# Optimization experiments

Measured on AMD Instinct MI355X. Metric: run time of the kernel, lower is better.

Reference implementation:

```python
import jax, jax.numpy as jnp
import numpy as np

N = 50000       # nodes
E = 800000      # edges (avg degree 16)
IN = 256        # input features
HEADS = 4
D = 32          # per-head dim (hidden_channels/heads = 128/4)
HID = HEADS * D # 128
OUT = 64        # out_channels, last layer has 1 head
SLOPE = 0.2     # DGL GATConv LeakyReLU negative slope


def setup_inputs() -> dict:
    key = jax.random.key(0)
    ks = jax.random.split(key, 11)
    s = 0.05
    return {
        "x": jax.random.normal(ks[0], (N, IN), jnp.float32),
        "W1": jax.random.normal(ks[1], (IN, HID), jnp.float32) * s,
        "al1": jax.random.normal(ks[2], (HEADS, D), jnp.float32) * s,
        "ar1": jax.random.normal(ks[3], (HEADS, D), jnp.float32) * s,
        "b1": jnp.zeros((HID,), jnp.float32),
        "W2": jax.random.normal(ks[4], (HID, OUT), jnp.float32) * s,
        "al2": jax.random.normal(ks[5], (1, OUT), jnp.float32) * s,
        "ar2": jax.random.normal(ks[6], (1, OUT), jnp.float32) * s,
        "b2": jnp.zeros((OUT,), jnp.float32),
        "src": jax.random.randint(ks[7], (E,), 0, N),
        "dst": jax.random.randint(ks[8], (E,), 0, N),
    }


def gat_conv(h, W, al, ar, b, src, dst, heads, d):
    # h: [N, F_in]; projects, computes edge attention, edge-softmax over dst,
    # scatter-reduce aggregation. Matches dglnn.GATConv (bias, no residual).
    feat = (h @ W).reshape(-1, heads, d)              # [N, H, D]
    el = jnp.einsum('nhd,hd->nh', feat, al)           # [N, H]
    er = jnp.einsum('nhd,hd->nh', feat, ar)           # [N, H]
    e = jax.nn.leaky_relu(el[src] + er[dst], SLOPE)   # [E, H] edge scores
    # edge softmax over incoming edges of each dst node
    m = jax.ops.segment_max(e, dst, num_segments=N)   # [N, H]
    ee = jnp.exp(e - m[dst])                          # [E, H]
    z = jax.ops.segment_sum(ee, dst, num_segments=N)  # [N, H]
    a = ee / z[dst]                                   # [E, H]
    msg = feat[src] * a[:, :, None]                   # [E, H, D] gather + weight
    out = jax.ops.segment_sum(msg, dst, num_segments=N)  # [N, H, D]
    return out + b.reshape(heads, d)


def reference(x, W1, al1, ar1, b1, W2, al2, ar2, b2, src, dst):
    h = gat_conv(x, W1, al1, ar1, b1, src, dst, HEADS, D)   # [N, 4, 32]
    h = jax.nn.relu(h).reshape(N, HID)                      # activation; dropout=identity (eval)
    h = gat_conv(h, W2, al2, ar2, b2, src, dst, 1, OUT)     # [N, 1, 64]
    return h.reshape(N, OUT)
```

## Files before the change

kernel.cpp:

```cpp
#include <hip/hip_runtime.h>
#include <math.h>

#define NN   50000
#define EE   800000
#define INF_ 256
#define HID  128
#define OUTF 64
#define DCAP 96
#define SLOPE 0.2f
#define G1B  782
#define NB   391
#define NCH  196
#define CHCAP 6144

typedef __attribute__((ext_vector_type(8))) short short8v;
typedef __attribute__((ext_vector_type(4))) float f32x4;

__device__ __forceinline__ float lrelu(float x) { return x > 0.f ? x : SLOPE * x; }
__device__ __forceinline__ float4 lrelu4(float4 v) {
  v.x = lrelu(v.x); v.y = lrelu(v.y); v.z = lrelu(v.z); v.w = lrelu(v.w); return v;
}
__device__ __forceinline__ unsigned short f2bf(float x) {
  unsigned int u = __float_as_uint(x);
  unsigned int r = (u + 0x7FFFu + ((u >> 16) & 1u)) >> 16;
  return (unsigned short)r;
}

__global__ __launch_bounds__(256) void prep_k(const int* __restrict__ src,
                                              const int* __restrict__ dst,
                                              int* __restrict__ cursor,
                                              int* __restrict__ packed,
                                              const float* __restrict__ W1,
                                              const float* __restrict__ W2,
                                              unsigned short* __restrict__ W1T,
                                              unsigned short* __restrict__ W2T) {
  int t = threadIdx.x;
  if (blockIdx.x >= NB) {
    int id = (blockIdx.x - NB) * 256 + t;
    if (id < 32768) {
      int k = id >> 7, c = id & 127;
      W1T[c * 256 + k] = f2bf(W1[k * 128 + c]);
    } else {
      int i2 = id - 32768;
      if (i2 < 8192) {
        int k = i2 >> 6, c = i2 & 63;
        W2T[c * 128 + k] = f2bf(W2[i2]);
      }
    }
    return;
  }
  __shared__ int h[NCH];
  __shared__ int cur[NCH];
  int b = blockIdx.x;
  if (t < NCH) h[t] = 0;
  __syncthreads();
  const int4* d4p = (const int4*)dst;
  const int4* s4p = (const int4*)src;
  int4 d4[2], s4[2];
  bool val[2];
#pragma unroll
  for (int it = 0; it < 2; ++it) {
    int qi = b * 512 + it * 256 + t;
    val[it] = qi < EE / 4;
    if (val[it]) {
      d4[it] = d4p[qi];
      s4[it] = s4p[qi];
      atomicAdd(&h[d4[it].x >> 8], 1);
      atomicAdd(&h[d4[it].y >> 8], 1);
      atomicAdd(&h[d4[it].z >> 8], 1);
      atomicAdd(&h[d4[it].w >> 8], 1);
    }
  }
  __syncthreads();
  if (t < NCH) {
    int c = h[t];
    cur[t] = t * CHCAP + ((c > 0) ? atomicAdd(&cursor[t], c) : 0);
  }
  __syncthreads();
#pragma unroll
  for (int it = 0; it < 2; ++it) {
    if (val[it]) {
      int p, c, lim;
      c = d4[it].x >> 8; lim = (c + 1) * CHCAP;
      p = atomicAdd(&cur[c], 1); if (p < lim) packed[p] = (s4[it].x << 8) | (d4[it].x & 255);
      c = d4[it].y >> 8; lim = (c + 1) * CHCAP;
      p = atomicAdd(&cur[c], 1); if (p < lim) packed[p] = (s4[it].y << 8) | (d4[it].y & 255);
      c = d4[it].z >> 8; lim = (c + 1) * CHCAP;
      p = atomicAdd(&cur[c], 1); if (p < lim) packed[p] = (s4[it].z << 8) | (d4[it].z & 255);
      c = d4[it].w >> 8; lim = (c + 1) * CHCAP;
      p = atomicAdd(&cur[c], 1); if (p < lim) packed[p] = (s4[it].w << 8) | (d4[it].w & 255);
    }
  }
}

__global__ __launch_bounds__(256) void cg1_k(const int* __restrict__ packed,
                                             const int* __restrict__ cursor,
                                             int* __restrict__ adj,
                                             int* __restrict__ rowptr,
                                             int* __restrict__ cnt,
                                             const float* __restrict__ x,
                                             const unsigned short* __restrict__ W1T,
                                             unsigned short* __restrict__ featb,
                                             const float* __restrict__ al,
                                             const float* __restrict__ ar,
                                             float* __restrict__ el,
                                             float* __restrict__ er) {
  __shared__ char smem[32768];
  int t = threadIdx.x;

  if (blockIdx.x < NCH) {
    int* pk  = (int*)smem;
    int* h   = (int*)(smem + 24576);
    int* sc  = (int*)(smem + 25600);
    int* cur = (int*)(smem + 26624);
    int b = blockIdx.x;
    int base = b * CHCAP;
    int len = cursor[b]; if (len > CHCAP) len = CHCAP;
    h[t] = 0;
    __syncthreads();
    for (int i = t; i < len; i += 256) {
      int v = packed[base + i];
      pk[i] = v;
      atomicAdd(&h[v & 255], 1);
    }
    __syncthreads();
    int v0 = h[t];
    sc[t] = v0;
    __syncthreads();
    for (int off = 1; off < 256; off <<= 1) {
      int add = (t >= off) ? sc[t - off] : 0;
      __syncthreads();
      sc[t] += add;
      __syncthreads();
    }
    int excl = sc[t] - v0;
    int node = b * 256 + t;
    if (node < NN) { cnt[node] = v0; rowptr[node] = base + excl; }
    cur[t] = excl;
    __syncthreads();
    for (int i = t; i < len; i += 256) {
      int v = pk[i];
      int p = atomicAdd(&cur[v & 255], 1);
      adj[base + p] = v & 0xFFFFFF00;
    }
    return;
  }

  unsigned short* As = (unsigned short*)smem;
  unsigned short* Bs = (unsigned short*)(smem + 16384);
  int lane = t & 63, wid = t >> 6;
  int n0 = (blockIdx.x - NCH) * 64;
  int wr = wid * 16;

  f32x4 acc[2][4];
#pragma unroll
  for (int m = 0; m < 2; ++m)
#pragma unroll
    for (int n = 0; n < 4; ++n) acc[m][n] = (f32x4){0.f, 0.f, 0.f, 0.f};

  for (int pass = 0; pass < 2; ++pass) {
    int k0 = pass * 128;
#pragma unroll
    for (int it = 0; it < 8; ++it) {
      int f = it * 256 + t;
      int row = f >> 5;
      int c4  = f & 31;
      int grow = n0 + row;
      float4 v = make_float4(0.f, 0.f, 0.f, 0.f);
      if (grow < NN) v = *(const float4*)&x[grow * INF_ + k0 + c4 * 4];
      ushort4 b4;
      b4.x = f2bf(v.x); b4.y = f2bf(v.y); b4.z = f2bf(v.z); b4.w = f2bf(v.w);
      int byte = row * 256 + c4 * 8;
      byte ^= (row & 15) << 4;
      *(ushort4*)((char*)As + byte) = b4;
    }
#pragma unroll
    for (int ch = 0; ch < 2; ++ch) {
#pragma unroll
      for (int it = 0; it < 4; ++it) {
        int f = it * 256 + t;
        int c  = f >> 4;
        int k8 = f & 15;
        uint4 v = *(const uint4*)&W1T[(ch * 64 + c) * 256 + k0 + k8 * 8];
        int byte = c * 256 + k8 * 16;
        byte ^= (c & 15) << 4;
        *(uint4*)((char*)Bs + byte) = v;
      }
      __syncthreads();
#pragma unroll
      for (int ks = 0; ks < 4; ++ks) {
        int kb = ks * 64 + (lane >> 4) * 16;
        int arow = wr + (lane & 15);
        int abyte = (arow * 256 + kb) ^ ((arow & 15) << 4);
        short8v a = *(const short8v*)((const char*)As + abyte);
#pragma unroll
        for (int n = 0; n < 4; ++n) {
          int c = n * 16 + (lane & 15);
          int bbyte = (c * 256 + kb) ^ ((c & 15) << 4);
          short8v b = *(const short8v*)((const char*)Bs + bbyte);
          acc[ch][n] = __builtin_amdgcn_mfma_f32_16x16x32_bf16(a, b, acc[ch][n], 0, 0, 0);
        }
      }
      __syncthreads();
    }
  }
#pragma unroll
  for (int ch = 0; ch < 2; ++ch) {
    int rbase = wr + (lane >> 4) * 4;
#pragma unroll
    for (int r = 0; r < 4; ++r)
#pragma unroll
      for (int n = 0; n < 4; ++n)
        As[(rbase + r) * 128 + ch * 64 + n * 16 + (lane & 15)] = f2bf(acc[ch][n][r]);
  }
  __syncthreads();
#pragma unroll
  for (int it = 0; it < 4; ++it) {
    int id = it * 256 + t;
    int row = id >> 4, c8 = id & 15;
    int grow = n0 + row;
    if (grow < NN)
      *(uint4*)&featb[grow * HID + c8 * 8] = *(const uint4*)&As[row * 128 + c8 * 8];
  }
  {
    int row = t >> 2, hh = t & 3;
    int grow = n0 + row;
    float pe = 0.f, pr = 0.f;
#pragma unroll
    for (int d = 0; d < 16; ++d) {
      unsigned int u = *(const unsigned int*)&As[row * 128 + hh * 32 + d * 2];
      float f0 = __uint_as_float(u << 16);
      float f1 = __uint_as_float(u & 0xFFFF0000u);
      float2 a2 = *(const float2*)&al[hh * 32 + d * 2];
      float2 r2 = *(const float2*)&ar[hh * 32 + d * 2];
      pe += f0 * a2.x + f1 * a2.y;
      pr += f0 * r2.x + f1 * r2.y;
    }
    if (grow < NN) { el[grow * 4 + hh] = pe; er[grow * 4 + hh] = pr; }
  }
}

__global__ __launch_bounds__(256) void agg1_k(const unsigned short* __restrict__ featb,
                                              const float* __restrict__ el1,
                                              const float* __restrict__ er1,
                                              const float* __restrict__ b1,
                                              const int* __restrict__ cnt,
                                              const int* __restrict__ rowptr,
                                              const int* __restrict__ adj,
                                              unsigned short* __restrict__ houtb) {
  __shared__ float ee[4][DCAP * 4];
  int wid = threadIdx.x >> 6, lane = threadIdx.x & 63;
  int n = blockIdx.x * 4 + wid;
  int deg = cnt[n]; if (deg > DCAP) deg = DCAP;
  const int* bk = adj + rowptr[n];
  float4 er = *(const float4*)(er1 + n * 4);
  int hl = lane >> 4;
  int m64 = deg < 64 ? deg : 64;
  int myoff = (lane < m64) ? bk[lane] : -1;
  const char* fb = (const char*)featb;
  int lb = lane * 4;

  float4 e4my = make_float4(0.f, 0.f, 0.f, 0.f);
  if (myoff >= 0 && deg <= 64)
    e4my = *(const float4*)((const char*)el1 + (myoff >> 4));
  unsigned int upre[16];
#pragma unroll
  for (int k = 0; k < 16; ++k) {
    int o = __shfl(myoff, k);
    upre[k] = *(const unsigned int*)(fb + ((k < m64) ? o : 0) + lb);
  }
  __builtin_amdgcn_sched_barrier(0);

  if (deg <= 64) {
    float4 ex = make_float4(0.f, 0.f, 0.f, 0.f);
    if (myoff >= 0) {
      float4 sc = lrelu4(make_float4(e4my.x + er.x, e4my.y + er.y,
                                     e4my.z + er.z, e4my.w + er.w));
      ex = make_float4(__expf(sc.x), __expf(sc.y), __expf(sc.z), __expf(sc.w));
    }
    float4 zs = ex;
#pragma unroll
    for (int off = 1; off < 64; off <<= 1) {
      zs.x += __shfl_xor(zs.x, off); zs.y += __shfl_xor(zs.y, off);
      zs.z += __shfl_xor(zs.z, off); zs.w += __shfl_xor(zs.w, off);
    }
    if (myoff >= 0) {
      float4 w = make_float4(ex.x / zs.x, ex.y / zs.y, ex.z / zs.z, ex.w / zs.w);
      *(float4*)&ee[wid][lane * 4] = w;
    }
  } else {
    float4 mx = make_float4(-INFINITY, -INFINITY, -INFINITY, -INFINITY);
    for (int j = lane; j < deg; j += 64) {
      int o = bk[j];
      float4 e4 = *(const float4*)((const char*)el1 + (o >> 4));
      float4 sc = lrelu4(make_float4(e4.x + er.x, e4.y + er.y, e4.z + er.z, e4.w + er.w));
      mx.x = fmaxf(mx.x, sc.x); mx.y = fmaxf(mx.y, sc.y);
      mx.z = fmaxf(mx.z, sc.z); mx.w = fmaxf(mx.w, sc.w);
    }
#pragma unroll
    for (int off = 1; off < 64; off <<= 1) {
      mx.x = fmaxf(mx.x, __shfl_xor(mx.x, off));
      mx.y = fmaxf(mx.y, __shfl_xor(mx.y, off));
      mx.z = fmaxf(mx.z, __shfl_xor(mx.z, off));
      mx.w = fmaxf(mx.w, __shfl_xor(mx.w, off));
    }
    float4 zs = make_float4(0.f, 0.f, 0.f, 0.f);
    for (int j = lane; j < deg; j += 64) {
      int o = bk[j];
      float4 e4 = *(const float4*)((const char*)el1 + (o >> 4));
      float4 sc = lrelu4(make_float4(e4.x + er.x, e4.y + er.y, e4.z + er.z, e4.w + er.w));
      float4 ex = make_float4(__expf(sc.x - mx.x), __expf(sc.y - mx.y),
                              __expf(sc.z - mx.z), __expf(sc.w - mx.w));
      *(float4*)&ee[wid][j * 4] = ex;
      zs.x += ex.x; zs.y += ex.y; zs.z += ex.z; zs.w += ex.w;
    }
#pragma unroll
    for (int off = 1; off < 64; off <<= 1) {
      zs.x += __shfl_xor(zs.x, off); zs.y += __shfl_xor(zs.y, off);
      zs.z += __shfl_xor(zs.z, off); zs.w += __shfl_xor(zs.w, off);
    }
    float4 iz = make_float4(1.f / zs.x, 1.f / zs.y, 1.f / zs.z, 1.f / zs.w);
    for (int j = lane; j < deg; j += 64) {
      float4 t = *(const float4*)&ee[wid][j * 4];
      t.x *= iz.x; t.y *= iz.y; t.z *= iz.z; t.w *= iz.w;
      *(float4*)&ee[wid][j * 4] = t;
    }
  }

  float acc0 = 0.f, acc1 = 0.f;
#pragma unroll
  for (int k = 0; k < 16; ++k) {
    float w = (k < m64) ? ee[wid][k * 4 + hl] : 0.f;
    acc0 += __uint_as_float(upre[k] << 16) * w;
    acc1 += __uint_as_float(upre[k] & 0xFFFF0000u) * w;
  }
  int j = 16;
  for (; j + 16 <= m64; j += 16) {
    unsigned int u[16];
#pragma unroll
    for (int q = 0; q < 16; ++q) {
      int o = __shfl(myoff, j + q);
      u[q] = *(const unsigned int*)(fb + o + lb);
    }
#pragma unroll
    for (int q = 0; q < 16; ++q) {
      float w = ee[wid][(j + q) * 4 + hl];
      acc0 += __uint_as_float(u[q] << 16) * w;
      acc1 += __uint_as_float(u[q] & 0xFFFF0000u) * w;
    }
  }
  for (; j + 4 <= m64; j += 4) {
    unsigned int u[4];
#pragma unroll
    for (int q = 0; q < 4; ++q) {
      int o = __shfl(myoff, j + q);
      u[q] = *(const unsigned int*)(fb + o + lb);
    }
#pragma unroll
    for (int q = 0; q < 4; ++q) {
      float w = ee[wid][(j + q) * 4 + hl];
      acc0 += __uint_as_float(u[q] << 16) * w;
      acc1 += __uint_as_float(u[q] & 0xFFFF0000u) * w;
    }
  }
  for (; j < m64; ++j) {
    int o = __shfl(myoff, j);
    unsigned int u = *(const unsigned int*)(fb + o + lb);
    float w = ee[wid][j * 4 + hl];
    acc0 += __uint_as_float(u << 16) * w; acc1 += __uint_as_float(u & 0xFFFF0000u) * w;
  }
  for (; j < deg; ++j) {
    int o = bk[j];
    unsigned int u = *(const unsigned int*)(fb + o + lb);
    float w = ee[wid][j * 4 + hl];
    acc0 += __uint_as_float(u << 16) * w; acc1 += __uint_as_float(u & 0xFFFF0000u) * w;
  }
  float2 bb = *(const float2*)&b1[lane * 2];
  float o0 = fmaxf(acc0 + bb.x, 0.f);
  float o1 = fmaxf(acc1 + bb.y, 0.f);
  unsigned int p = (unsigned int)f2bf(o0) | ((unsigned int)f2bf(o1) << 16);
  *(unsigned int*)&houtb[n * HID + lane * 2] = p;
}

__global__ __launch_bounds__(256) void gemm2s_mfma(const unsigned short* __restrict__ hb,
                                                   const unsigned short* __restrict__ W2T,
                                                   unsigned short* __restrict__ f2b,
                                                   const float* __restrict__ al2,
                                                   const float* __restrict__ ar2,
                                                   float* __restrict__ el2,
                                                   float* __restrict__ er2) {
  __shared__ char smem[32768];
  __shared__ float pel[64][4], per_[64][4];
  unsigned short* As = (unsigned short*)smem;
  unsigned short* Bs = (unsigned short*)(smem + 16384);
  int t = threadIdx.x, lane = t & 63, wid = t >> 6;
  int n0 = blockIdx.x * 64;
  f32x4 acc[4];
#pragma unroll
  for (int n = 0; n < 4; ++n) acc[n] = (f32x4){0.f, 0.f, 0.f, 0.f};

#pragma unroll
  for (int it = 0; it < 4; ++it) {
    int id = it * 256 + t;
    int row = id >> 4, c8 = id & 15;
    int grow = n0 + row;
    uint4 v = make_uint4(0, 0, 0, 0);
    if (grow < NN) v = *(const uint4*)&hb[grow * HID + c8 * 8];
    int byte = row * 256 + c8 * 16;
    byte ^= (row & 15) << 4;
    *(uint4*)((char*)As + byte) = v;
  }
#pragma unroll
  for (int it = 0; it < 4; ++it) {
    int id = it * 256 + t;
    int row = id >> 4, c8 = id & 15;
    uint4 v = *(const uint4*)&W2T[row * 128 + c8 * 8];
    int byte = row * 256 + c8 * 16;
    byte ^= (row & 15) << 4;
    *(uint4*)((char*)Bs + byte) = v;
  }
  __syncthreads();
  int wr = wid * 16;
#pragma unroll
  for (int ks = 0; ks < 4; ++ks) {
    int kb = ks * 64 + (lane >> 4) * 16;
    int arow = wr + (lane & 15);
    int abyte = (arow * 256 + kb) ^ ((arow & 15) << 4);
    short8v a = *(const short8v*)((const char*)As + abyte);
#pragma unroll
    for (int n = 0; n < 4; ++n) {
      int c = n * 16 + (lane & 15);
      int bbyte = (c * 256 + kb) ^ ((c & 15) << 4);
      short8v b = *(const short8v*)((const char*)Bs + bbyte);
      acc[n] = __builtin_amdgcn_mfma_f32_16x16x32_bf16(a, b, acc[n], 0, 0, 0);
    }
  }
  __syncthreads();
  float* stg = (float*)smem;
  unsigned short* sB = (unsigned short*)(smem + 16640);
  int rloc = wr + (lane >> 4) * 4;
#pragma unroll
  for (int r = 0; r < 4; ++r) {
#pragma unroll
    for (int n = 0; n < 4; ++n) {
      int col = n * 16 + (lane & 15);
      float v = acc[n][r];
      stg[(rloc + r) * 65 + col] = v;
      sB[(rloc + r) * 64 + col] = f2bf(v);
    }
  }
  __syncthreads();
#pragma unroll
  for (int it = 0; it < 2; ++it) {
    int id = it * 256 + t;
    int row = id >> 3, c8 = id & 7;
    int grow = n0 + row;
    if (grow < NN)
      *(uint4*)&f2b[grow * OUTF + c8 * 8] = *(const uint4*)&sB[row * 64 + c8 * 8];
  }
  {
    int row = t >> 2, seg = t & 3;
    float pe = 0.f, pr = 0.f;
#pragma unroll
    for (int d = 0; d < 16; ++d) {
      int c = seg * 16 + d;
      float f = stg[row * 65 + c];
      pe += f * al2[c];
      pr += f * ar2[c];
    }
    pel[row][seg] = pe; per_[row][seg] = pr;
  }
  __syncthreads();
  if (t < 64) {
    int grow = n0 + t;
    if (grow < NN) {
      el2[grow] = pel[t][0] + pel[t][1] + pel[t][2] + pel[t][3];
      er2[grow] = per_[t][0] + per_[t][1] + per_[t][2] + per_[t][3];
    }
  }
}

__global__ __launch_bounds__(256) void agg2_k(const unsigned short* __restrict__ f2b,
                                              const float* __restrict__ el2,
                                              const float* __restrict__ er2,
                                              const float* __restrict__ b2,
                                              const int* __restrict__ cnt,
                                              const int* __restrict__ rowptr,
                                              const int* __restrict__ adj,
                                              float* __restrict__ out) {
  __shared__ float ee[4][DCAP];
  int wid = threadIdx.x >> 6, lane = threadIdx.x & 63;
  int n = blockIdx.x * 4 + wid;
  int deg = cnt[n]; if (deg > DCAP) deg = DCAP;
  const int* bk = adj + rowptr[n];
  float er = er2[n];
  int m64 = deg < 64 ? deg : 64;
  int myoff = (lane < m64) ? bk[lane] : -1;
  int half = lane >> 5, c2 = (lane & 31) * 2;
  const char* fb = (const char*)f2b;

  float elmy = 0.f;
  if (myoff >= 0 && deg <= 64)
    elmy = *(const float*)((const char*)el2 + (myoff >> 6));
  unsigned int upre[8];
#pragma unroll
  for (int s = 0; s < 8; ++s) {
    int je = s * 2 + half;
    int o = __shfl(myoff, je);
    upre[s] = *(const unsigned int*)(fb + ((je < m64) ? (o >> 1) : 0) + c2 * 2);
  }
  __builtin_amdgcn_sched_barrier(0);

  if (deg <= 64) {
    float ex = (myoff >= 0) ? __expf(lrelu(elmy + er)) : 0.f;
    float zs = ex;
#pragma unroll
    for (int off = 1; off < 64; off <<= 1) zs += __shfl_xor(zs, off);
    if (myoff >= 0) ee[wid][lane] = ex / zs;
  } else {
    float mx = -INFINITY;
    for (int j = lane; j < deg; j += 64) {
      int o = bk[j];
      mx = fmaxf(mx, lrelu(*(const float*)((const char*)el2 + (o >> 6)) + er));
    }
#pragma unroll
    for (int off = 1; off < 64; off <<= 1) mx = fmaxf(mx, __shfl_xor(mx, off));
    float zs = 0.f;
    for (int j = lane; j < deg; j += 64) {
      int o = bk[j];
      float ex = __expf(lrelu(*(const float*)((const char*)el2 + (o >> 6)) + er) - mx);
      ee[wid][j] = ex;
      zs += ex;
    }
#pragma unroll
    for (int off = 1; off < 64; off <<= 1) zs += __shfl_xor(zs, off);
    float iz = 1.f / zs;
    for (int j = lane; j < deg; j += 64) ee[wid][j] *= iz;
  }

  float acc0 = 0.f, acc1 = 0.f;
#pragma unroll
  for (int s = 0; s < 8; ++s) {
    int je = s * 2 + half;
    float w = (je < m64) ? ee[wid][je] : 0.f;
    acc0 += __uint_as_float(upre[s] << 16) * w;
    acc1 += __uint_as_float(upre[s] & 0xFFFF0000u) * w;
  }
  int j = 16;
  for (; j + 16 <= deg; j += 16) {
    unsigned int u[8]; float w[8];
#pragma unroll
    for (int q = 0; q < 8; ++q) {
      int je = j + q * 2 + half;
      int os = __shfl(myoff, je < 64 ? je : 63);
      int o = (je < 64) ? os : bk[je];
      u[q] = *(const unsigned int*)(fb + (o >> 1) + c2 * 2);
      w[q] = ee[wid][je];
    }
#pragma unroll
    for (int q = 0; q < 8; ++q) {
      acc0 += __uint_as_float(u[q] << 16) * w[q];
      acc1 += __uint_as_float(u[q] & 0xFFFF0000u) * w[q];
    }
  }
  for (; j < deg; j += 2) {
    int je = j + half;
    int os = __shfl(myoff, (je < 64) ? je : 63);
    float w = 0.f; unsigned int u = 0;
    if (je < deg) {
      int o = (je < 64) ? os : bk[je];
      u = *(const unsigned int*)(fb + (o >> 1) + c2 * 2);
      w = ee[wid][je];
    }
    acc0 += __uint_as_float(u << 16) * w;
    acc1 += __uint_as_float(u & 0xFFFF0000u) * w;
  }
  acc0 += __shfl_xor(acc0, 32);
  acc1 += __shfl_xor(acc1, 32);
  if (lane < 32) {
    float2 bb = *(const float2*)&b2[c2];
    *(float2*)&out[n * OUTF + c2] = make_float2(acc0 + bb.x, acc1 + bb.y);
  }
}

extern "C" void kernel_launch(void* const* d_in, const int* in_sizes, int n_in,
                              void* d_out, int out_size, void* d_ws, size_t ws_size,
                              hipStream_t stream) {
  const float* x   = (const float*)d_in[0];
  const float* W1  = (const float*)d_in[1];
  const float* al1 = (const float*)d_in[2];
  const float* ar1 = (const float*)d_in[3];
  const float* b1  = (const float*)d_in[4];
  const float* W2  = (const float*)d_in[5];
  const float* al2 = (const float*)d_in[6];
  const float* ar2 = (const float*)d_in[7];
  const float* b2  = (const float*)d_in[8];
  const int*   src = (const int*)d_in[9];
  const int*   dst = (const int*)d_in[10];
  float* out = (float*)d_out;

  char* base = (char*)d_ws;
  unsigned short* feat1b = (unsigned short*)base;
  unsigned short* f2b    = (unsigned short*)base;
  unsigned short* hb     = (unsigned short*)(base + 12800000);
  float* el1 = (float*)(base + 25600000);
  float* er1 = el1 + NN * 4;
  float* el2 = er1 + NN * 4;
  float* er2 = el2 + NN;
  int* cnt    = (int*)(er2 + NN);
  int* rowptr = cnt + NN;
  int* adj    = rowptr + NN;
  int* packed = adj + NCH * CHCAP;
  int* cursor = packed + NCH * CHCAP;
  unsigned short* W1T = (unsigned short*)(cursor + NCH);
  unsigned short* W2T = W1T + 256 * 128;

  hipMemsetAsync(cursor, 0, NCH * sizeof(int), stream);
  prep_k <<<NB + 161, 256, 0, stream>>>(src, dst, cursor, packed, W1, W2, W1T, W2T);
  cg1_k  <<<NCH + G1B, 256, 0, stream>>>(packed, cursor, adj, rowptr, cnt,
                                         x, W1T, feat1b, al1, ar1, el1, er1);
  agg1_k <<<NN / 4, 256, 0, stream>>>(feat1b, el1, er1, b1, cnt, rowptr, adj, hb);
  gemm2s_mfma<<<G1B, 256, 0, stream>>>(hb, W2T, f2b, al2, ar2, el2, er2);
  agg2_k <<<NN / 4, 256, 0, stream>>>(f2b, el2, er2, b2, cnt, rowptr, adj, out);
}
```

Before: 115.5 us.

## Shrink layer-1 GEMM tile to 32 rows and read W1T fragments from global

The layer-1 projection in cg1_k now handles 32 rows per block instead of 64. It stages the full 256-wide K slice of x once, and each of the four waves computes a 16x64 quadrant. B fragments are read directly from global/L2 instead of being staged through shared memory, which removes the Bs buffer and several barriers and doubles the block count. The trade-off is repeated uncoalesced W1T reads per wave (relying on cache) and redundant x-tile setup per block. The gemm2 grid is rewritten as an expression that gives the same value as before.

```diff
diff --git a/kernel.cpp b/kernel.cpp
--- a/kernel.cpp
+++ b/kernel.cpp
@@ -8,10 +8,10 @@
 #define OUTF 64
 #define DCAP 96
 #define SLOPE 0.2f
-#define G1B  782
 #define NB   391
 #define NCH  196
 #define CHCAP 6144
+#define G1B32 1563
 
 typedef __attribute__((ext_vector_type(8))) short short8v;
 typedef __attribute__((ext_vector_type(4))) float f32x4;
@@ -147,82 +147,63 @@
   }
 
   unsigned short* As = (unsigned short*)smem;
-  unsigned short* Bs = (unsigned short*)(smem + 16384);
   int lane = t & 63, wid = t >> 6;
-  int n0 = (blockIdx.x - NCH) * 64;
-  int wr = wid * 16;
-
-  f32x4 acc[2][4];
-#pragma unroll
-  for (int m = 0; m < 2; ++m)
-#pragma unroll
-    for (int n = 0; n < 4; ++n) acc[m][n] = (f32x4){0.f, 0.f, 0.f, 0.f};
-
-  for (int pass = 0; pass < 2; ++pass) {
-    int k0 = pass * 128;
-#pragma unroll
-    for (int it = 0; it < 8; ++it) {
-      int f = it * 256 + t;
-      int row = f >> 5;
-      int c4  = f & 31;
-      int grow = n0 + row;
-      float4 v = make_float4(0.f, 0.f, 0.f, 0.f);
-      if (grow < NN) v = *(const float4*)&x[grow * INF_ + k0 + c4 * 4];
-      ushort4 b4;
-      b4.x = f2bf(v.x); b4.y = f2bf(v.y); b4.z = f2bf(v.z); b4.w = f2bf(v.w);
-      int byte = row * 256 + c4 * 8;
-      byte ^= (row & 15) << 4;
-      *(ushort4*)((char*)As + byte) = b4;
-    }
-#pragma unroll
-    for (int ch = 0; ch < 2; ++ch) {
-#pragma unroll
-      for (int it = 0; it < 4; ++it) {
-        int f = it * 256 + t;
-        int c  = f >> 4;
-        int k8 = f & 15;
-        uint4 v = *(const uint4*)&W1T[(ch * 64 + c) * 256 + k0 + k8 * 8];
-        int byte = c * 256 + k8 * 16;
-        byte ^= (c & 15) << 4;
-        *(uint4*)((char*)Bs + byte) = v;
-      }
-      __syncthreads();
-#pragma unroll
-      for (int ks = 0; ks < 4; ++ks) {
-        int kb = ks * 64 + (lane >> 4) * 16;
-        int arow = wr + (lane & 15);
-        int abyte = (arow * 256 + kb) ^ ((arow & 15) << 4);
-        short8v a = *(const short8v*)((const char*)As + abyte);
-#pragma unroll
-        for (int n = 0; n < 4; ++n) {
-          int c = n * 16 + (lane & 15);
-          int bbyte = (c * 256 + kb) ^ ((c & 15) << 4);
-          short8v b = *(const short8v*)((const char*)Bs + bbyte);
-          acc[ch][n] = __builtin_amdgcn_mfma_f32_16x16x32_bf16(a, b, acc[ch][n], 0, 0, 0);
-        }
-      }
-      __syncthreads();
-    }
-  }
-#pragma unroll
-  for (int ch = 0; ch < 2; ++ch) {
+  int n0 = (blockIdx.x - NCH) * 32;
+  int wr = (wid & 1) * 16;
+  int wc = (wid >> 1) * 64;
+
+#pragma unroll
+  for (int it = 0; it < 8; ++it) {
+    int f = it * 256 + t;
+    int row = f >> 6;
+    int c4  = f & 63;
+    int grow = n0 + row;
+    float4 v = make_float4(0.f, 0.f, 0.f, 0.f);
+    if (grow < NN) v = *(const float4*)&x[grow * INF_ + c4 * 4];
+    ushort4 b4;
+    b4.x = f2bf(v.x); b4.y = f2bf(v.y); b4.z = f2bf(v.z); b4.w = f2bf(v.w);
+    int byte = row * 512 + c4 * 8;
+    byte ^= (row & 15) << 4;
+    *(ushort4*)((char*)As + byte) = b4;
+  }
+  __syncthreads();
+
+  f32x4 acc[4];
+#pragma unroll
+  for (int n = 0; n < 4; ++n) acc[n] = (f32x4){0.f, 0.f, 0.f, 0.f};
+  const char* wb = (const char*)W1T;
+#pragma unroll
+  for (int ks = 0; ks < 8; ++ks) {
+    int kbyte = ks * 64 + (lane >> 4) * 16;
+    int arow = wr + (lane & 15);
+    int abyte = (arow * 512 + kbyte) ^ ((arow & 15) << 4);
+    short8v a = *(const short8v*)((const char*)As + abyte);
+#pragma unroll
+    for (int n = 0; n < 4; ++n) {
+      int c = wc + n * 16 + (lane & 15);
+      short8v b = *(const short8v*)(wb + c * 512 + kbyte);
+      acc[n] = __builtin_amdgcn_mfma_f32_16x16x32_bf16(a, b, acc[n], 0, 0, 0);
+    }
+  }
+  __syncthreads();
+  {
     int rbase = wr + (lane >> 4) * 4;
 #pragma unroll
     for (int r = 0; r < 4; ++r)
 #pragma unroll
       for (int n = 0; n < 4; ++n)
-        As[(rbase + r) * 128 + ch * 64 + n * 16 + (lane & 15)] = f2bf(acc[ch][n][r]);
-  }
-  __syncthreads();
-#pragma unroll
-  for (int it = 0; it < 4; ++it) {
+        As[(rbase + r) * 128 + wc + n * 16 + (lane & 15)] = f2bf(acc[n][r]);
+  }
+  __syncthreads();
+#pragma unroll
+  for (int it = 0; it < 2; ++it) {
     int id = it * 256 + t;
     int row = id >> 4, c8 = id & 15;
     int grow = n0 + row;
     if (grow < NN)
       *(uint4*)&featb[grow * HID + c8 * 8] = *(const uint4*)&As[row * 128 + c8 * 8];
   }
-  {
+  if (t < 128) {
     int row = t >> 2, hh = t & 3;
     int grow = n0 + row;
     float pe = 0.f, pr = 0.f;
@@ -617,9 +598,9 @@
 
   hipMemsetAsync(cursor, 0, NCH * sizeof(int), stream);
   prep_k <<<NB + 161, 256, 0, stream>>>(src, dst, cursor, packed, W1, W2, W1T, W2T);
-  cg1_k  <<<NCH + G1B, 256, 0, stream>>>(packed, cursor, adj, rowptr, cnt,
-                                         x, W1T, feat1b, al1, ar1, el1, er1);
+  cg1_k  <<<NCH + G1B32, 256, 0, stream>>>(packed, cursor, adj, rowptr, cnt,
+                                           x, W1T, feat1b, al1, ar1, el1, er1);
   agg1_k <<<NN / 4, 256, 0, stream>>>(feat1b, el1, er1, b1, cnt, rowptr, adj, hb);
-  gemm2s_mfma<<<G1B, 256, 0, stream>>>(hb, W2T, f2b, al2, ar2, el2, er2);
+  gemm2s_mfma<<<(NN + 63) / 64, 256, 0, stream>>>(hb, W2T, f2b, al2, ar2, el2, er2);
   agg2_k <<<NN / 4, 256, 0, stream>>>(f2b, el2, er2, b2, cnt, rowptr, adj, out);
 }
```

Result: slower. 130.1 us (+12.7%).
